# Kernel optimization log

Measured on AMD Instinct MI355X. Metric: run time of the kernel, lower is better.

## Reference

```python
import jax, jax.numpy as jnp
import numpy as np

EMBED_DIM = 1024
NUM_HEADS = 16
HEAD_DIM = EMBED_DIM // NUM_HEADS


def setup_inputs() -> dict:
    key = jax.random.key(0)
    kx, kw1, kb1, kw2, kb2 = jax.random.split(key, 5)
    B, T, C = 4, 2048, EMBED_DIM
    s = 1.0 / np.sqrt(C)
    return {
        "x": jax.random.normal(kx, (B, T, C), dtype=jnp.float32),
        "qkv_w": jax.random.uniform(kw1, (3 * C, C), jnp.float32, -s, s),
        "qkv_b": jax.random.uniform(kb1, (3 * C,), jnp.float32, -s, s),
        "out_w": jax.random.uniform(kw2, (C, C), jnp.float32, -s, s),
        "out_b": jax.random.uniform(kb2, (C,), jnp.float32, -s, s),
    }


def reference(x, qkv_w, qkv_b, out_w, out_b):
    B, T, C = x.shape
    H, D = NUM_HEADS, HEAD_DIM
    qkv = x @ qkv_w.T + qkv_b                      # [B,T,3C]
    qkv = qkv.reshape(B, T, 3, H, D)
    q = qkv[:, :, 0].transpose(0, 2, 1, 3)         # [B,H,T,D]
    k = qkv[:, :, 1].transpose(0, 2, 1, 3)
    v = qkv[:, :, 2].transpose(0, 2, 1, 3)
    att = jnp.einsum("bhqd,bhkd->bhqk", q, k) / jnp.sqrt(jnp.float32(D))
    causal = jnp.tril(jnp.ones((T, T), dtype=bool))
    att = jnp.where(causal, att, -jnp.inf)
    att = jax.nn.softmax(att, axis=-1)
    out = jnp.einsum("bhqk,bhkd->bhqd", att, v)    # [B,H,T,D]
    out = out.transpose(0, 2, 1, 3).reshape(B, T, C)
    return out @ out_w.T + out_b
```

## Files before the change

kernel.cpp:

```cpp
#include <hip/hip_runtime.h>
#include <stdint.h>

typedef _Float16 f16;
typedef _Float16 f16x2 __attribute__((ext_vector_type(2)));
typedef _Float16 f16x4 __attribute__((ext_vector_type(4)));
typedef _Float16 f16x8 __attribute__((ext_vector_type(8)));
typedef float f32x4 __attribute__((ext_vector_type(4)));
typedef float f32x16 __attribute__((ext_vector_type(16)));
typedef unsigned int u32;
typedef unsigned int u32x4 __attribute__((ext_vector_type(4)));
typedef int i32x2 __attribute__((ext_vector_type(2)));

#define LOG2E 1.44269504088896340736f

__device__ __forceinline__ f32x4 mfma_16x16x32(f16x8 a, f16x8 b, f32x4 c) {
    return __builtin_amdgcn_mfma_f32_16x16x32_f16(a, b, c, 0, 0, 0);
}
__device__ __forceinline__ f32x16 mfma_32x32x16(f16x8 a, f16x8 b, f32x16 c) {
    return __builtin_amdgcn_mfma_f32_32x32x16_f16(a, b, c, 0, 0, 0);
}

__device__ __forceinline__ void gload_lds16(const void* g, void* l) {
    __builtin_amdgcn_global_load_lds(
        (const __attribute__((address_space(1))) unsigned int*)g,
        (__attribute__((address_space(3))) unsigned int*)l, 16, 0, 0);
}

__device__ __forceinline__ void plswap_u32(u32& a, u32& b) {
    i32x2 r = __builtin_amdgcn_permlane32_swap((int)a, (int)b, false, false);
    a = (u32)r[0]; b = (u32)r[1];
}

__global__ void cast_f32_f16(const float* __restrict__ src, f16* __restrict__ dst, int n4) {
    int i = blockIdx.x * 256 + threadIdx.x;
    if (i >= n4) return;
    float4 v = reinterpret_cast<const float4*>(src)[i];
    f16x4 o;
    o[0] = (f16)v.x; o[1] = (f16)v.y; o[2] = (f16)v.z; o[3] = (f16)v.w;
    reinterpret_cast<f16x4*>(dst)[i] = o;
}

template<int MODE>
__global__ __launch_bounds__(256, 2)
void gemm_tn(const f16* __restrict__ A, const f16* __restrict__ W,
             const float* __restrict__ bias, void* __restrict__ outp,
             int M, int N, int K)
{
    __shared__ __align__(16) f16 As[128 * 32];
    __shared__ __align__(16) f16 Bs[128 * 32];

    const int lane = threadIdx.x & 63;
    const int wave = threadIdx.x >> 6;
    const int l15 = lane & 15, l4 = lane >> 4;

    const int nwg = (int)(gridDim.x * gridDim.y);
    int orig = (int)(blockIdx.y * gridDim.x + blockIdx.x);
    int cpx = nwg >> 3;
    int w = (orig & 7) * cpx + (orig >> 3);
    const int row0 = (w / (int)gridDim.x) * 128;
    const int col0 = (w % (int)gridDim.x) * 128;
    const int wr = wave >> 1, wc = wave & 1;

    f32x4 acc[4][4] = {};

    const int srow = lane >> 2;
    const int scol = (lane & 3) * 8;

    for (int k0 = 0; k0 < K; k0 += 32) {
        __syncthreads();
        #pragma unroll
        for (int it = 0; it < 2; ++it) {
            int chunk = it * 4 + wave;
            const f16* gA = A + (size_t)(row0 + chunk * 16 + srow) * K + k0 + scol;
            gload_lds16(gA, As + chunk * 512);
            const f16* gB = W + (size_t)(col0 + chunk * 16 + srow) * K + k0 + scol;
            gload_lds16(gB, Bs + chunk * 512);
        }
        __syncthreads();

        f16x8 af[4], bf[4];
        #pragma unroll
        for (int m = 0; m < 4; ++m)
            af[m] = *reinterpret_cast<const f16x8*>(As + (wr * 64 + m * 16 + l15) * 32 + l4 * 8);
        #pragma unroll
        for (int n = 0; n < 4; ++n)
            bf[n] = *reinterpret_cast<const f16x8*>(Bs + (wc * 64 + n * 16 + l15) * 32 + l4 * 8);
        #pragma unroll
        for (int m = 0; m < 4; ++m)
            #pragma unroll
            for (int n = 0; n < 4; ++n)
                acc[m][n] = mfma_16x16x32(af[m], bf[n], acc[m][n]);
    }

    if (MODE == 0) {
        f16* qb = (f16*)outp;
        const size_t HS = (size_t)64 * 2048 * 64;
        #pragma unroll
        for (int m = 0; m < 4; ++m) {
            int rbase = row0 + wr * 64 + m * 16 + l4 * 4;
            #pragma unroll
            for (int n = 0; n < 4; ++n) {
                int j = col0 + wc * 64 + n * 16 + l15;
                int which = j >> 10;
                int h = (j >> 6) & 15;
                int d = j & 63;
                float bj = bias[j];
                f16* base = qb + (size_t)which * HS;
                float scale = (which == 0) ? (0.125f * LOG2E) : 1.0f;
                #pragma unroll
                for (int r = 0; r < 4; ++r) {
                    int row = rbase + r;
                    int b = row >> 11, t = row & 2047;
                    size_t off = ((size_t)(b * 16 + h) * 2048 + t) * 64 + d;
                    base[off] = (f16)((acc[m][n][r] + bj) * scale);
                }
            }
        }
    } else {
        float* O = (float*)outp;
        #pragma unroll
        for (int m = 0; m < 4; ++m) {
            int rbase = row0 + wr * 64 + m * 16 + l4 * 4;
            #pragma unroll
            for (int n = 0; n < 4; ++n) {
                int j = col0 + wc * 64 + n * 16 + l15;
                float bj = bias[j];
                #pragma unroll
                for (int r = 0; r < 4; ++r)
                    O[(size_t)(rbase + r) * N + j] = acc[m][n][r] + bj;
            }
        }
    }
}

__global__ __launch_bounds__(256, 4)
void attn_kernel(const f16* __restrict__ qb, const f16* __restrict__ kb,
                 const f16* __restrict__ vb, f16* __restrict__ ob)
{
    __shared__ __align__(16) f16 Ks[2][4096];
    __shared__ __align__(16) f16 Vs[2][64][68];

    const int tid = (int)threadIdx.x;
    const int bh = (int)blockIdx.x;
    const int qblk = (int)gridDim.y - 1 - (int)blockIdx.y;
    const int lane = tid & 63;
    const int wave = tid >> 6;
    const int l31 = lane & 31;
    const int hi  = lane >> 5;
    const int q0 = qblk * 128;
    const int qw = q0 + wave * 32;

    const f16* Qp = qb + ((size_t)bh * 2048 + qw) * 64;
    f16x8 qf[4];
    #pragma unroll
    for (int ss = 0; ss < 4; ++ss)
        qf[ss] = *reinterpret_cast<const f16x8*>(Qp + l31 * 64 + ss * 16 + hi * 8);

    float Lr = 0.0f;
    f32x16 oacc[2] = {};

    const int ntiles = 2 * qblk + 2;
    const f16* Kbh = kb + (size_t)bh * 2048 * 64;
    const f16* Vbh = vb + (size_t)bh * 2048 * 64;

    f16x8 vld0, vld1;
    {
        #pragma unroll
        for (int it = 0; it < 2; ++it) {
            int c = it * 4 + wave;
            gload_lds16(Kbh + lane * 64 + c * 8, &Ks[0][0] + c * 512);
        }
        vld0 = *reinterpret_cast<const f16x8*>(Vbh + lane * 64 + (wave * 2 + 0) * 8);
        vld1 = *reinterpret_cast<const f16x8*>(Vbh + lane * 64 + (wave * 2 + 1) * 8);
    }

    for (int t = 0; t < ntiles; ++t) {
        const int cur = t & 1;
        const int kv0 = t * 64;

        #pragma unroll
        for (int it = 0; it < 2; ++it) {
            int dblk = wave * 2 + it;
            const f16x8 v = it ? vld1 : vld0;
            #pragma unroll
            for (int e = 0; e < 8; ++e)
                Vs[cur][dblk * 8 + e][lane] = v[e];
        }

        __syncthreads();

        {
            const int kvn = (t + 1 < ntiles) ? (t + 1) * 64 : t * 64;
            const f16* Ktn = Kbh + (size_t)kvn * 64;
            #pragma unroll
            for (int it = 0; it < 2; ++it) {
                int c = it * 4 + wave;
                gload_lds16(Ktn + lane * 64 + c * 8, &Ks[cur ^ 1][0] + c * 512);
            }
            const f16* Vtn = Vbh + (size_t)kvn * 64;
            vld0 = *reinterpret_cast<const f16x8*>(Vtn + lane * 64 + (wave * 2 + 0) * 8);
            vld1 = *reinterpret_cast<const f16x8*>(Vtn + lane * 64 + (wave * 2 + 1) * 8);
        }

        if (kv0 <= qw + 31) {
            const f16* Ksc = &Ks[cur][0];

            f32x16 s0 = {}, s1 = {};
            __builtin_amdgcn_s_setprio(1);
            #pragma unroll
            for (int ss = 0; ss < 4; ++ss) {
                f16x8 kf0 = *reinterpret_cast<const f16x8*>(Ksc + (2 * ss + hi) * 512 + l31 * 8);
                f16x8 kf1 = *reinterpret_cast<const f16x8*>(Ksc + (2 * ss + hi) * 512 + (32 + l31) * 8);
                s0 = mfma_32x32x16(kf0, qf[ss], s0);
                s1 = mfma_32x32x16(kf1, qf[ss], s1);
            }
            __builtin_amdgcn_s_setprio(0);

            if (kv0 + 63 > qw) {
                const int qg = qw + l31;
                #pragma unroll
                for (int r = 0; r < 16; ++r) {
                    int k0g = kv0 + (r & 3) + 8 * (r >> 2) + 4 * hi;
                    if (k0g > qg)      s0[r] = -1e30f;
                    if (k0g + 32 > qg) s1[r] = -1e30f;
                }
            }

            float e0[16], e1[16];
            #pragma unroll
            for (int r = 0; r < 16; ++r) {
                e0[r] = exp2f(s0[r] - 8.0f);
                e1[r] = exp2f(s1[r] - 8.0f);
            }
            float sm[16];
            #pragma unroll
            for (int i = 0; i < 16; ++i) sm[i] = e0[i] + e1[i];
            #pragma unroll
            for (int st = 8; st > 0; st >>= 1)
                #pragma unroll
                for (int i = 0; i < st; ++i) sm[i] += sm[i + st];
            float rs = sm[0];
            rs += __shfl_xor(rs, 32);
            Lr += rs;

            u32 cpk[2][8];
            #pragma unroll
            for (int B = 0; B < 4; ++B) {
                cpk[0][2 * B]     = __builtin_bit_cast(u32, __builtin_amdgcn_cvt_pkrtz(e0[4 * B],     e0[4 * B + 1]));
                cpk[0][2 * B + 1] = __builtin_bit_cast(u32, __builtin_amdgcn_cvt_pkrtz(e0[4 * B + 2], e0[4 * B + 3]));
                cpk[1][2 * B]     = __builtin_bit_cast(u32, __builtin_amdgcn_cvt_pkrtz(e1[4 * B],     e1[4 * B + 1]));
                cpk[1][2 * B + 1] = __builtin_bit_cast(u32, __builtin_amdgcn_cvt_pkrtz(e1[4 * B + 2], e1[4 * B + 3]));
            }

            __builtin_amdgcn_s_setprio(1);
            #pragma unroll
            for (int ss = 0; ss < 4; ++ss) {
                const int kbi = ss >> 1, qq = ss & 1;
                u32 a0 = cpk[kbi][4 * qq + 0], b0 = cpk[kbi][4 * qq + 2];
                u32 a1 = cpk[kbi][4 * qq + 1], b1 = cpk[kbi][4 * qq + 3];
                plswap_u32(a0, b0);
                plswap_u32(a1, b1);
                u32x4 up; up[0] = a0; up[1] = a1; up[2] = b0; up[3] = b1;
                f16x8 pa = __builtin_bit_cast(f16x8, up);
                #pragma unroll
                for (int db = 0; db < 2; ++db) {
                    const f16* vp = &Vs[cur][db * 32 + l31][16 * ss + 8 * hi];
                    f16x4 v0 = *reinterpret_cast<const f16x4*>(vp);
                    f16x4 v1 = *reinterpret_cast<const f16x4*>(vp + 4);
                    f16x8 vf = __builtin_shufflevector(v0, v1, 0, 1, 2, 3, 4, 5, 6, 7);
                    oacc[db] = mfma_32x32x16(pa, vf, oacc[db]);
                }
            }
            __builtin_amdgcn_s_setprio(0);
        }
    }

    float rcp = 1.0f / Lr;
    float rr[16];
    #pragma unroll
    for (int r = 0; r < 16; ++r)
        rr[r] = __shfl(rcp, (r & 3) + 8 * (r >> 2) + 4 * hi);

    const int b = bh >> 4, h = bh & 15;
    f16* O = ob + ((size_t)b * 2048 + qw) * 1024 + h * 64;
    #pragma unroll
    for (int db = 0; db < 2; ++db)
        #pragma unroll
        for (int r = 0; r < 16; ++r) {
            int q = (r & 3) + 8 * (r >> 2) + 4 * hi;
            O[(size_t)q * 1024 + db * 32 + l31] = (f16)(oacc[db][r] * rr[r]);
        }
}

extern "C" void kernel_launch(void* const* d_in, const int* in_sizes, int n_in,
                              void* d_out, int out_size, void* d_ws, size_t ws_size,
                              hipStream_t stream)
{
    const float* x    = (const float*)d_in[0];
    const float* qkvw = (const float*)d_in[1];
    const float* qkvb = (const float*)d_in[2];
    const float* outw = (const float*)d_in[3];
    const float* outb = (const float*)d_in[4];
    float* out = (float*)d_out;

    f16* x_h    = (f16*)d_ws;
    f16* qkvw_h = x_h + (size_t)8192 * 1024;
    f16* outw_h = qkvw_h + (size_t)3072 * 1024;
    f16* q_buf  = outw_h + (size_t)1024 * 1024;
    f16* att_o  = q_buf + (size_t)3 * 8388608;

    cast_f32_f16<<<8192, 256, 0, stream>>>(x, x_h, 2097152);
    cast_f32_f16<<<3072, 256, 0, stream>>>(qkvw, qkvw_h, 786432);
    cast_f32_f16<<<1024, 256, 0, stream>>>(outw, outw_h, 262144);

    gemm_tn<0><<<dim3(24, 64), 256, 0, stream>>>(x_h, qkvw_h, qkvb, q_buf, 8192, 3072, 1024);
    attn_kernel<<<dim3(64, 16), 256, 0, stream>>>(q_buf, q_buf + 8388608, q_buf + 2 * 8388608, att_o);
    gemm_tn<1><<<dim3(8, 64), 256, 0, stream>>>(att_o, outw_h, outb, out, 8192, 1024, 1024);
}
```

Baseline: 188.2 us.

## Pair low and high causal query blocks per attention workgroup; fuse cast kernels

Each attention workgroup now handles two query blocks, p and 15-p, so every block does the same amount of causal work. Both blocks share the K/V tiles already staged in LDS, which halves K/V loads per query and removes the tail imbalance. The cost is roughly double the accumulator and Q register use, so occupancy drops from 4 to 2 blocks per CU, and the grid shrinks to 512 blocks. The three fp32-to-fp16 cast launches are also merged into one kernel that picks its source by block index.

```diff
diff --git a/kernel.cpp b/kernel.cpp
--- a/kernel.cpp
+++ b/kernel.cpp
@@ -31,9 +31,16 @@
     a = (u32)r[0]; b = (u32)r[1];
 }
 
-__global__ void cast_f32_f16(const float* __restrict__ src, f16* __restrict__ dst, int n4) {
-    int i = blockIdx.x * 256 + threadIdx.x;
-    if (i >= n4) return;
+__global__ void cast_all(const float* __restrict__ x, const float* __restrict__ w1,
+                         const float* __restrict__ w2, f16* __restrict__ xo,
+                         f16* __restrict__ w1o, f16* __restrict__ w2o) {
+    int b = blockIdx.x;
+    const float* src;
+    f16* dst;
+    int i;
+    if (b < 8192)       { src = x;  dst = xo;  i = b * 256 + (int)threadIdx.x; }
+    else if (b < 11264) { src = w1; dst = w1o; i = (b - 8192) * 256 + (int)threadIdx.x; }
+    else                { src = w2; dst = w2o; i = (b - 11264) * 256 + (int)threadIdx.x; }
     float4 v = reinterpret_cast<const float4*>(src)[i];
     f16x4 o;
     o[0] = (f16)v.x; o[1] = (f16)v.y; o[2] = (f16)v.z; o[3] = (f16)v.w;
@@ -133,7 +140,7 @@
     }
 }
 
-__global__ __launch_bounds__(256, 4)
+__global__ __launch_bounds__(256, 2)
 void attn_kernel(const f16* __restrict__ qb, const f16* __restrict__ kb,
                  const f16* __restrict__ vb, f16* __restrict__ ob)
 {
@@ -142,24 +149,28 @@
 
     const int tid = (int)threadIdx.x;
     const int bh = (int)blockIdx.x;
-    const int qblk = (int)gridDim.y - 1 - (int)blockIdx.y;
+    const int p = (int)blockIdx.y;
+    const int qlo = p, qhi = 15 - p;
     const int lane = tid & 63;
     const int wave = tid >> 6;
     const int l31 = lane & 31;
     const int hi  = lane >> 5;
-    const int q0 = qblk * 128;
-    const int qw = q0 + wave * 32;
-
-    const f16* Qp = qb + ((size_t)bh * 2048 + qw) * 64;
-    f16x8 qf[4];
+
+    const int qwlo = qlo * 128 + wave * 32;
+    const int qwhi = qhi * 128 + wave * 32;
+
+    const f16* Qbh = qb + (size_t)bh * 2048 * 64;
+    f16x8 qflo[4], qfhi[4];
     #pragma unroll
-    for (int ss = 0; ss < 4; ++ss)
-        qf[ss] = *reinterpret_cast<const f16x8*>(Qp + l31 * 64 + ss * 16 + hi * 8);
-
-    float Lr = 0.0f;
-    f32x16 oacc[2] = {};
-
-    const int ntiles = 2 * qblk + 2;
+    for (int ss = 0; ss < 4; ++ss) {
+        qflo[ss] = *reinterpret_cast<const f16x8*>(Qbh + (size_t)(qwlo + l31) * 64 + ss * 16 + hi * 8);
+        qfhi[ss] = *reinterpret_cast<const f16x8*>(Qbh + (size_t)(qwhi + l31) * 64 + ss * 16 + hi * 8);
+    }
+
+    float Llo = 0.0f, Lhi = 0.0f;
+    f32x16 olo[2] = {}, ohi[2] = {};
+
+    const int ntiles = 2 * qhi + 2;
     const f16* Kbh = kb + (size_t)bh * 2048 * 64;
     const f16* Vbh = vb + (size_t)bh * 2048 * 64;
 
@@ -202,22 +213,34 @@
             vld1 = *reinterpret_cast<const f16x8*>(Vtn + lane * 64 + (wave * 2 + 1) * 8);
         }
 
-        if (kv0 <= qw + 31) {
-            const f16* Ksc = &Ks[cur][0];
-
-            f32x16 s0 = {}, s1 = {};
-            __builtin_amdgcn_s_setprio(1);
-            #pragma unroll
-            for (int ss = 0; ss < 4; ++ss) {
-                f16x8 kf0 = *reinterpret_cast<const f16x8*>(Ksc + (2 * ss + hi) * 512 + l31 * 8);
-                f16x8 kf1 = *reinterpret_cast<const f16x8*>(Ksc + (2 * ss + hi) * 512 + (32 + l31) * 8);
-                s0 = mfma_32x32x16(kf0, qf[ss], s0);
-                s1 = mfma_32x32x16(kf1, qf[ss], s1);
-            }
-            __builtin_amdgcn_s_setprio(0);
-
-            if (kv0 + 63 > qw) {
-                const int qg = qw + l31;
+        const bool do_hi = (kv0 <= qwhi + 31);
+        const bool do_lo = (kv0 <= qwlo + 31);
+        if (!(do_hi || do_lo)) continue;
+
+        const f16* Ksc = &Ks[cur][0];
+
+        f32x16 sh0 = {}, sh1 = {}, sl0 = {}, sl1 = {};
+        __builtin_amdgcn_s_setprio(1);
+        #pragma unroll
+        for (int ss = 0; ss < 4; ++ss) {
+            f16x8 kf0 = *reinterpret_cast<const f16x8*>(Ksc + (2 * ss + hi) * 512 + l31 * 8);
+            f16x8 kf1 = *reinterpret_cast<const f16x8*>(Ksc + (2 * ss + hi) * 512 + (32 + l31) * 8);
+            if (do_hi) {
+                sh0 = mfma_32x32x16(kf0, qfhi[ss], sh0);
+                sh1 = mfma_32x32x16(kf1, qfhi[ss], sh1);
+            }
+            if (do_lo) {
+                sl0 = mfma_32x32x16(kf0, qflo[ss], sl0);
+                sl1 = mfma_32x32x16(kf1, qflo[ss], sl1);
+            }
+        }
+        __builtin_amdgcn_s_setprio(0);
+
+        u32 cpkh[2][8], cpkl[2][8];
+        auto softmax_pack = [&](f32x16& s0, f32x16& s1, float& Lr,
+                                int qbase, u32 (&cpk)[2][8]) {
+            if (kv0 + 63 > qbase) {
+                const int qg = qbase + l31;
                 #pragma unroll
                 for (int r = 0; r < 16; ++r) {
                     int k0g = kv0 + (r & 3) + 8 * (r >> 2) + 4 * hi;
@@ -225,7 +248,6 @@
                     if (k0g + 32 > qg) s1[r] = -1e30f;
                 }
             }
-
             float e0[16], e1[16];
             #pragma unroll
             for (int r = 0; r < 16; ++r) {
@@ -242,8 +264,6 @@
             float rs = sm[0];
             rs += __shfl_xor(rs, 32);
             Lr += rs;
-
-            u32 cpk[2][8];
             #pragma unroll
             for (int B = 0; B < 4; ++B) {
                 cpk[0][2 * B]     = __builtin_bit_cast(u32, __builtin_amdgcn_cvt_pkrtz(e0[4 * B],     e0[4 * B + 1]));
@@ -251,45 +271,75 @@
                 cpk[1][2 * B]     = __builtin_bit_cast(u32, __builtin_amdgcn_cvt_pkrtz(e1[4 * B],     e1[4 * B + 1]));
                 cpk[1][2 * B + 1] = __builtin_bit_cast(u32, __builtin_amdgcn_cvt_pkrtz(e1[4 * B + 2], e1[4 * B + 3]));
             }
-
-            __builtin_amdgcn_s_setprio(1);
-            #pragma unroll
-            for (int ss = 0; ss < 4; ++ss) {
-                const int kbi = ss >> 1, qq = ss & 1;
-                u32 a0 = cpk[kbi][4 * qq + 0], b0 = cpk[kbi][4 * qq + 2];
-                u32 a1 = cpk[kbi][4 * qq + 1], b1 = cpk[kbi][4 * qq + 3];
+        };
+        if (do_hi) softmax_pack(sh0, sh1, Lhi, qwhi, cpkh);
+        if (do_lo) softmax_pack(sl0, sl1, Llo, qwlo, cpkl);
+
+        __builtin_amdgcn_s_setprio(1);
+        #pragma unroll
+        for (int ss = 0; ss < 4; ++ss) {
+            const int kbi = ss >> 1, qq = ss & 1;
+            f16x8 pah, pal;
+            if (do_hi) {
+                u32 a0 = cpkh[kbi][4 * qq + 0], b0 = cpkh[kbi][4 * qq + 2];
+                u32 a1 = cpkh[kbi][4 * qq + 1], b1 = cpkh[kbi][4 * qq + 3];
                 plswap_u32(a0, b0);
                 plswap_u32(a1, b1);
                 u32x4 up; up[0] = a0; up[1] = a1; up[2] = b0; up[3] = b1;
-                f16x8 pa = __builtin_bit_cast(f16x8, up);
-                #pragma unroll
-                for (int db = 0; db < 2; ++db) {
-                    const f16* vp = &Vs[cur][db * 32 + l31][16 * ss + 8 * hi];
-                    f16x4 v0 = *reinterpret_cast<const f16x4*>(vp);
-                    f16x4 v1 = *reinterpret_cast<const f16x4*>(vp + 4);
-                    f16x8 vf = __builtin_shufflevector(v0, v1, 0, 1, 2, 3, 4, 5, 6, 7);
-                    oacc[db] = mfma_32x32x16(pa, vf, oacc[db]);
-                }
-            }
-            __builtin_amdgcn_s_setprio(0);
-        }
-    }
-
-    float rcp = 1.0f / Lr;
-    float rr[16];
-    #pragma unroll
-    for (int r = 0; r < 16; ++r)
-        rr[r] = __shfl(rcp, (r & 3) + 8 * (r >> 2) + 4 * hi);
+                pah = __builtin_bit_cast(f16x8, up);
+            }
+            if (do_lo) {
+                u32 a0 = cpkl[kbi][4 * qq + 0], b0 = cpkl[kbi][4 * qq + 2];
+                u32 a1 = cpkl[kbi][4 * qq + 1], b1 = cpkl[kbi][4 * qq + 3];
+                plswap_u32(a0, b0);
+                plswap_u32(a1, b1);
+                u32x4 up; up[0] = a0; up[1] = a1; up[2] = b0; up[3] = b1;
+                pal = __builtin_bit_cast(f16x8, up);
+            }
+            #pragma unroll
+            for (int db = 0; db < 2; ++db) {
+                const f16* vp = &Vs[cur][db * 32 + l31][16 * ss + 8 * hi];
+                f16x4 v0 = *reinterpret_cast<const f16x4*>(vp);
+                f16x4 v1 = *reinterpret_cast<const f16x4*>(vp + 4);
+                f16x8 vf = __builtin_shufflevector(v0, v1, 0, 1, 2, 3, 4, 5, 6, 7);
+                if (do_hi) ohi[db] = mfma_32x32x16(pah, vf, ohi[db]);
+                if (do_lo) olo[db] = mfma_32x32x16(pal, vf, olo[db]);
+            }
+        }
+        __builtin_amdgcn_s_setprio(0);
+    }
 
     const int b = bh >> 4, h = bh & 15;
-    f16* O = ob + ((size_t)b * 2048 + qw) * 1024 + h * 64;
-    #pragma unroll
-    for (int db = 0; db < 2; ++db)
-        #pragma unroll
-        for (int r = 0; r < 16; ++r) {
-            int q = (r & 3) + 8 * (r >> 2) + 4 * hi;
-            O[(size_t)q * 1024 + db * 32 + l31] = (f16)(oacc[db][r] * rr[r]);
-        }
+    {
+        float rcp = 1.0f / Lhi;
+        float rr[16];
+        #pragma unroll
+        for (int r = 0; r < 16; ++r)
+            rr[r] = __shfl(rcp, (r & 3) + 8 * (r >> 2) + 4 * hi);
+        f16* O = ob + ((size_t)b * 2048 + qwhi) * 1024 + h * 64;
+        #pragma unroll
+        for (int db = 0; db < 2; ++db)
+            #pragma unroll
+            for (int r = 0; r < 16; ++r) {
+                int q = (r & 3) + 8 * (r >> 2) + 4 * hi;
+                O[(size_t)q * 1024 + db * 32 + l31] = (f16)(ohi[db][r] * rr[r]);
+            }
+    }
+    {
+        float rcp = 1.0f / Llo;
+        float rr[16];
+        #pragma unroll
+        for (int r = 0; r < 16; ++r)
+            rr[r] = __shfl(rcp, (r & 3) + 8 * (r >> 2) + 4 * hi);
+        f16* O = ob + ((size_t)b * 2048 + qwlo) * 1024 + h * 64;
+        #pragma unroll
+        for (int db = 0; db < 2; ++db)
+            #pragma unroll
+            for (int r = 0; r < 16; ++r) {
+                int q = (r & 3) + 8 * (r >> 2) + 4 * hi;
+                O[(size_t)q * 1024 + db * 32 + l31] = (f16)(olo[db][r] * rr[r]);
+            }
+    }
 }
 
 extern "C" void kernel_launch(void* const* d_in, const int* in_sizes, int n_in,
@@ -309,11 +359,9 @@
     f16* q_buf  = outw_h + (size_t)1024 * 1024;
     f16* att_o  = q_buf + (size_t)3 * 8388608;
 
-    cast_f32_f16<<<8192, 256, 0, stream>>>(x, x_h, 2097152);
-    cast_f32_f16<<<3072, 256, 0, stream>>>(qkvw, qkvw_h, 786432);
-    cast_f32_f16<<<1024, 256, 0, stream>>>(outw, outw_h, 262144);
+    cast_all<<<12288, 256, 0, stream>>>(x, qkvw, outw, x_h, qkvw_h, outw_h);
 
     gemm_tn<0><<<dim3(24, 64), 256, 0, stream>>>(x_h, qkvw_h, qkvb, q_buf, 8192, 3072, 1024);
-    attn_kernel<<<dim3(64, 16), 256, 0, stream>>>(q_buf, q_buf + 8388608, q_buf + 2 * 8388608, att_o);
+    attn_kernel<<<dim3(64, 8), 256, 0, stream>>>(q_buf, q_buf + 8388608, q_buf + 2 * 8388608, att_o);
     gemm_tn<1><<<dim3(8, 64), 256, 0, stream>>>(att_o, outw_h, outb, out, 8192, 1024, 1024);
 }
```

After: 195.4 us. 1.04x slower.

## Use persistent attention blocks with atomic work queue and fuse cast kernels

Applied to the files above, without the earlier changes.

The attention kernel becomes persistent: 768 blocks pull (q-block, head) jobs from a global atomic counter in order of longest causal work first, which balances the triangular workload across CUs. The three fp32-to-fp16 cast launches are merged into one kernel, and a memset resets the counter each call. The redundant prefetch on the last tile is also skipped. This adds an atomic and a barrier per job and one extra memset launch, and there is a possible LDS race when the next job's first K load overwrites buffer 0 while slow waves may still be reading it.

```diff
diff --git a/kernel.cpp b/kernel.cpp
--- a/kernel.cpp
+++ b/kernel.cpp
@@ -31,9 +31,16 @@
     a = (u32)r[0]; b = (u32)r[1];
 }
 
-__global__ void cast_f32_f16(const float* __restrict__ src, f16* __restrict__ dst, int n4) {
-    int i = blockIdx.x * 256 + threadIdx.x;
-    if (i >= n4) return;
+__global__ void cast_all(const float* __restrict__ x, const float* __restrict__ w1,
+                         const float* __restrict__ w2, f16* __restrict__ xo,
+                         f16* __restrict__ w1o, f16* __restrict__ w2o) {
+    int b = blockIdx.x;
+    const float* src;
+    f16* dst;
+    int i;
+    if (b < 8192)       { src = x;  dst = xo;  i = b * 256 + (int)threadIdx.x; }
+    else if (b < 11264) { src = w1; dst = w1o; i = (b - 8192) * 256 + (int)threadIdx.x; }
+    else                { src = w2; dst = w2o; i = (b - 11264) * 256 + (int)threadIdx.x; }
     float4 v = reinterpret_cast<const float4*>(src)[i];
     f16x4 o;
     o[0] = (f16)v.x; o[1] = (f16)v.y; o[2] = (f16)v.z; o[3] = (f16)v.w;
@@ -135,161 +142,171 @@
 
 __global__ __launch_bounds__(256, 4)
 void attn_kernel(const f16* __restrict__ qb, const f16* __restrict__ kb,
-                 const f16* __restrict__ vb, f16* __restrict__ ob)
+                 const f16* __restrict__ vb, f16* __restrict__ ob,
+                 u32* __restrict__ counter)
 {
     __shared__ __align__(16) f16 Ks[2][4096];
     __shared__ __align__(16) f16 Vs[2][64][68];
+    __shared__ int s_job;
 
     const int tid = (int)threadIdx.x;
-    const int bh = (int)blockIdx.x;
-    const int qblk = (int)gridDim.y - 1 - (int)blockIdx.y;
     const int lane = tid & 63;
     const int wave = tid >> 6;
     const int l31 = lane & 31;
     const int hi  = lane >> 5;
-    const int q0 = qblk * 128;
-    const int qw = q0 + wave * 32;
-
-    const f16* Qp = qb + ((size_t)bh * 2048 + qw) * 64;
-    f16x8 qf[4];
-    #pragma unroll
-    for (int ss = 0; ss < 4; ++ss)
-        qf[ss] = *reinterpret_cast<const f16x8*>(Qp + l31 * 64 + ss * 16 + hi * 8);
-
-    float Lr = 0.0f;
-    f32x16 oacc[2] = {};
-
-    const int ntiles = 2 * qblk + 2;
-    const f16* Kbh = kb + (size_t)bh * 2048 * 64;
-    const f16* Vbh = vb + (size_t)bh * 2048 * 64;
-
-    f16x8 vld0, vld1;
-    {
-        #pragma unroll
-        for (int it = 0; it < 2; ++it) {
-            int c = it * 4 + wave;
-            gload_lds16(Kbh + lane * 64 + c * 8, &Ks[0][0] + c * 512);
-        }
-        vld0 = *reinterpret_cast<const f16x8*>(Vbh + lane * 64 + (wave * 2 + 0) * 8);
-        vld1 = *reinterpret_cast<const f16x8*>(Vbh + lane * 64 + (wave * 2 + 1) * 8);
-    }
-
-    for (int t = 0; t < ntiles; ++t) {
-        const int cur = t & 1;
-        const int kv0 = t * 64;
-
-        #pragma unroll
-        for (int it = 0; it < 2; ++it) {
-            int dblk = wave * 2 + it;
-            const f16x8 v = it ? vld1 : vld0;
-            #pragma unroll
-            for (int e = 0; e < 8; ++e)
-                Vs[cur][dblk * 8 + e][lane] = v[e];
-        }
-
+
+    for (;;) {
+        if (tid == 0) s_job = (int)atomicAdd(counter, 1u);
         __syncthreads();
-
+        const int j = s_job;
+        if (j >= 1024) return;
+
+        const int qblk = 15 - (j >> 6);
+        const int bh = j & 63;
+        const int q0 = qblk * 128;
+        const int qw = q0 + wave * 32;
+
+        const f16* Qp = qb + ((size_t)bh * 2048 + qw) * 64;
+        f16x8 qf[4];
+        #pragma unroll
+        for (int ss = 0; ss < 4; ++ss)
+            qf[ss] = *reinterpret_cast<const f16x8*>(Qp + l31 * 64 + ss * 16 + hi * 8);
+
+        float Lr = 0.0f;
+        f32x16 oacc[2] = {};
+
+        const int ntiles = 2 * qblk + 2;
+        const f16* Kbh = kb + (size_t)bh * 2048 * 64;
+        const f16* Vbh = vb + (size_t)bh * 2048 * 64;
+
+        f16x8 vld0, vld1;
         {
-            const int kvn = (t + 1 < ntiles) ? (t + 1) * 64 : t * 64;
-            const f16* Ktn = Kbh + (size_t)kvn * 64;
             #pragma unroll
             for (int it = 0; it < 2; ++it) {
                 int c = it * 4 + wave;
-                gload_lds16(Ktn + lane * 64 + c * 8, &Ks[cur ^ 1][0] + c * 512);
-            }
-            const f16* Vtn = Vbh + (size_t)kvn * 64;
-            vld0 = *reinterpret_cast<const f16x8*>(Vtn + lane * 64 + (wave * 2 + 0) * 8);
-            vld1 = *reinterpret_cast<const f16x8*>(Vtn + lane * 64 + (wave * 2 + 1) * 8);
-        }
-
-        if (kv0 <= qw + 31) {
-            const f16* Ksc = &Ks[cur][0];
-
-            f32x16 s0 = {}, s1 = {};
-            __builtin_amdgcn_s_setprio(1);
-            #pragma unroll
-            for (int ss = 0; ss < 4; ++ss) {
-                f16x8 kf0 = *reinterpret_cast<const f16x8*>(Ksc + (2 * ss + hi) * 512 + l31 * 8);
-                f16x8 kf1 = *reinterpret_cast<const f16x8*>(Ksc + (2 * ss + hi) * 512 + (32 + l31) * 8);
-                s0 = mfma_32x32x16(kf0, qf[ss], s0);
-                s1 = mfma_32x32x16(kf1, qf[ss], s1);
-            }
-            __builtin_amdgcn_s_setprio(0);
-
-            if (kv0 + 63 > qw) {
-                const int qg = qw + l31;
+                gload_lds16(Kbh + lane * 64 + c * 8, &Ks[0][0] + c * 512);
+            }
+            vld0 = *reinterpret_cast<const f16x8*>(Vbh + lane * 64 + (wave * 2 + 0) * 8);
+            vld1 = *reinterpret_cast<const f16x8*>(Vbh + lane * 64 + (wave * 2 + 1) * 8);
+        }
+
+        for (int t = 0; t < ntiles; ++t) {
+            const int cur = t & 1;
+            const int kv0 = t * 64;
+
+            #pragma unroll
+            for (int it = 0; it < 2; ++it) {
+                int dblk = wave * 2 + it;
+                const f16x8 v = it ? vld1 : vld0;
+                #pragma unroll
+                for (int e = 0; e < 8; ++e)
+                    Vs[cur][dblk * 8 + e][lane] = v[e];
+            }
+
+            __syncthreads();
+
+            if (t + 1 < ntiles) {
+                const int kvn = (t + 1) * 64;
+                const f16* Ktn = Kbh + (size_t)kvn * 64;
+                #pragma unroll
+                for (int it = 0; it < 2; ++it) {
+                    int c = it * 4 + wave;
+                    gload_lds16(Ktn + lane * 64 + c * 8, &Ks[cur ^ 1][0] + c * 512);
+                }
+                const f16* Vtn = Vbh + (size_t)kvn * 64;
+                vld0 = *reinterpret_cast<const f16x8*>(Vtn + lane * 64 + (wave * 2 + 0) * 8);
+                vld1 = *reinterpret_cast<const f16x8*>(Vtn + lane * 64 + (wave * 2 + 1) * 8);
+            }
+
+            if (kv0 <= qw + 31) {
+                const f16* Ksc = &Ks[cur][0];
+
+                f32x16 s0 = {}, s1 = {};
+                __builtin_amdgcn_s_setprio(1);
+                #pragma unroll
+                for (int ss = 0; ss < 4; ++ss) {
+                    f16x8 kf0 = *reinterpret_cast<const f16x8*>(Ksc + (2 * ss + hi) * 512 + l31 * 8);
+                    f16x8 kf1 = *reinterpret_cast<const f16x8*>(Ksc + (2 * ss + hi) * 512 + (32 + l31) * 8);
+                    s0 = mfma_32x32x16(kf0, qf[ss], s0);
+                    s1 = mfma_32x32x16(kf1, qf[ss], s1);
+                }
+                __builtin_amdgcn_s_setprio(0);
+
+                if (kv0 + 63 > qw) {
+                    const int qg = qw + l31;
+                    #pragma unroll
+                    for (int r = 0; r < 16; ++r) {
+                        int k0g = kv0 + (r & 3) + 8 * (r >> 2) + 4 * hi;
+                        if (k0g > qg)      s0[r] = -1e30f;
+                        if (k0g + 32 > qg) s1[r] = -1e30f;
+                    }
+                }
+
+                float e0[16], e1[16];
                 #pragma unroll
                 for (int r = 0; r < 16; ++r) {
-                    int k0g = kv0 + (r & 3) + 8 * (r >> 2) + 4 * hi;
-                    if (k0g > qg)      s0[r] = -1e30f;
-                    if (k0g + 32 > qg) s1[r] = -1e30f;
-                }
-            }
-
-            float e0[16], e1[16];
+                    e0[r] = exp2f(s0[r] - 8.0f);
+                    e1[r] = exp2f(s1[r] - 8.0f);
+                }
+                float sm[16];
+                #pragma unroll
+                for (int i = 0; i < 16; ++i) sm[i] = e0[i] + e1[i];
+                #pragma unroll
+                for (int st = 8; st > 0; st >>= 1)
+                    #pragma unroll
+                    for (int i = 0; i < st; ++i) sm[i] += sm[i + st];
+                float rs = sm[0];
+                rs += __shfl_xor(rs, 32);
+                Lr += rs;
+
+                u32 cpk[2][8];
+                #pragma unroll
+                for (int B = 0; B < 4; ++B) {
+                    cpk[0][2 * B]     = __builtin_bit_cast(u32, __builtin_amdgcn_cvt_pkrtz(e0[4 * B],     e0[4 * B + 1]));
+                    cpk[0][2 * B + 1] = __builtin_bit_cast(u32, __builtin_amdgcn_cvt_pkrtz(e0[4 * B + 2], e0[4 * B + 3]));
+                    cpk[1][2 * B]     = __builtin_bit_cast(u32, __builtin_amdgcn_cvt_pkrtz(e1[4 * B],     e1[4 * B + 1]));
+                    cpk[1][2 * B + 1] = __builtin_bit_cast(u32, __builtin_amdgcn_cvt_pkrtz(e1[4 * B + 2], e1[4 * B + 3]));
+                }
+
+                __builtin_amdgcn_s_setprio(1);
+                #pragma unroll
+                for (int ss = 0; ss < 4; ++ss) {
+                    const int kbi = ss >> 1, qq = ss & 1;
+                    u32 a0 = cpk[kbi][4 * qq + 0], b0 = cpk[kbi][4 * qq + 2];
+                    u32 a1 = cpk[kbi][4 * qq + 1], b1 = cpk[kbi][4 * qq + 3];
+                    plswap_u32(a0, b0);
+                    plswap_u32(a1, b1);
+                    u32x4 up; up[0] = a0; up[1] = a1; up[2] = b0; up[3] = b1;
+                    f16x8 pa = __builtin_bit_cast(f16x8, up);
+                    #pragma unroll
+                    for (int db = 0; db < 2; ++db) {
+                        const f16* vp = &Vs[cur][db * 32 + l31][16 * ss + 8 * hi];
+                        f16x4 v0 = *reinterpret_cast<const f16x4*>(vp);
+                        f16x4 v1 = *reinterpret_cast<const f16x4*>(vp + 4);
+                        f16x8 vf = __builtin_shufflevector(v0, v1, 0, 1, 2, 3, 4, 5, 6, 7);
+                        oacc[db] = mfma_32x32x16(pa, vf, oacc[db]);
+                    }
+                }
+                __builtin_amdgcn_s_setprio(0);
+            }
+        }
+
+        float rcp = 1.0f / Lr;
+        float rr[16];
+        #pragma unroll
+        for (int r = 0; r < 16; ++r)
+            rr[r] = __shfl(rcp, (r & 3) + 8 * (r >> 2) + 4 * hi);
+
+        const int b = bh >> 4, h = bh & 15;
+        f16* O = ob + ((size_t)b * 2048 + qw) * 1024 + h * 64;
+        #pragma unroll
+        for (int db = 0; db < 2; ++db)
             #pragma unroll
             for (int r = 0; r < 16; ++r) {
-                e0[r] = exp2f(s0[r] - 8.0f);
-                e1[r] = exp2f(s1[r] - 8.0f);
-            }
-            float sm[16];
-            #pragma unroll
-            for (int i = 0; i < 16; ++i) sm[i] = e0[i] + e1[i];
-            #pragma unroll
-            for (int st = 8; st > 0; st >>= 1)
-                #pragma unroll
-                for (int i = 0; i < st; ++i) sm[i] += sm[i + st];
-            float rs = sm[0];
-            rs += __shfl_xor(rs, 32);
-            Lr += rs;
-
-            u32 cpk[2][8];
-            #pragma unroll
-            for (int B = 0; B < 4; ++B) {
-                cpk[0][2 * B]     = __builtin_bit_cast(u32, __builtin_amdgcn_cvt_pkrtz(e0[4 * B],     e0[4 * B + 1]));
-                cpk[0][2 * B + 1] = __builtin_bit_cast(u32, __builtin_amdgcn_cvt_pkrtz(e0[4 * B + 2], e0[4 * B + 3]));
-                cpk[1][2 * B]     = __builtin_bit_cast(u32, __builtin_amdgcn_cvt_pkrtz(e1[4 * B],     e1[4 * B + 1]));
-                cpk[1][2 * B + 1] = __builtin_bit_cast(u32, __builtin_amdgcn_cvt_pkrtz(e1[4 * B + 2], e1[4 * B + 3]));
-            }
-
-            __builtin_amdgcn_s_setprio(1);
-            #pragma unroll
-            for (int ss = 0; ss < 4; ++ss) {
-                const int kbi = ss >> 1, qq = ss & 1;
-                u32 a0 = cpk[kbi][4 * qq + 0], b0 = cpk[kbi][4 * qq + 2];
-                u32 a1 = cpk[kbi][4 * qq + 1], b1 = cpk[kbi][4 * qq + 3];
-                plswap_u32(a0, b0);
-                plswap_u32(a1, b1);
-                u32x4 up; up[0] = a0; up[1] = a1; up[2] = b0; up[3] = b1;
-                f16x8 pa = __builtin_bit_cast(f16x8, up);
-                #pragma unroll
-                for (int db = 0; db < 2; ++db) {
-                    const f16* vp = &Vs[cur][db * 32 + l31][16 * ss + 8 * hi];
-                    f16x4 v0 = *reinterpret_cast<const f16x4*>(vp);
-                    f16x4 v1 = *reinterpret_cast<const f16x4*>(vp + 4);
-                    f16x8 vf = __builtin_shufflevector(v0, v1, 0, 1, 2, 3, 4, 5, 6, 7);
-                    oacc[db] = mfma_32x32x16(pa, vf, oacc[db]);
-                }
-            }
-            __builtin_amdgcn_s_setprio(0);
-        }
+                int q = (r & 3) + 8 * (r >> 2) + 4 * hi;
+                O[(size_t)q * 1024 + db * 32 + l31] = (f16)(oacc[db][r] * rr[r]);
+            }
     }
-
-    float rcp = 1.0f / Lr;
-    float rr[16];
-    #pragma unroll
-    for (int r = 0; r < 16; ++r)
-        rr[r] = __shfl(rcp, (r & 3) + 8 * (r >> 2) + 4 * hi);
-
-    const int b = bh >> 4, h = bh & 15;
-    f16* O = ob + ((size_t)b * 2048 + qw) * 1024 + h * 64;
-    #pragma unroll
-    for (int db = 0; db < 2; ++db)
-        #pragma unroll
-        for (int r = 0; r < 16; ++r) {
-            int q = (r & 3) + 8 * (r >> 2) + 4 * hi;
-            O[(size_t)q * 1024 + db * 32 + l31] = (f16)(oacc[db][r] * rr[r]);
-        }
 }
 
 extern "C" void kernel_launch(void* const* d_in, const int* in_sizes, int n_in,
@@ -308,12 +325,12 @@
     f16* outw_h = qkvw_h + (size_t)3072 * 1024;
     f16* q_buf  = outw_h + (size_t)1024 * 1024;
     f16* att_o  = q_buf + (size_t)3 * 8388608;
-
-    cast_f32_f16<<<8192, 256, 0, stream>>>(x, x_h, 2097152);
-    cast_f32_f16<<<3072, 256, 0, stream>>>(qkvw, qkvw_h, 786432);
-    cast_f32_f16<<<1024, 256, 0, stream>>>(outw, outw_h, 262144);
+    u32* counter = (u32*)(att_o + (size_t)8192 * 1024);
+
+    hipMemsetAsync(counter, 0, 4, stream);
+    cast_all<<<12288, 256, 0, stream>>>(x, qkvw, outw, x_h, qkvw_h, outw_h);
 
     gemm_tn<0><<<dim3(24, 64), 256, 0, stream>>>(x_h, qkvw_h, qkvb, q_buf, 8192, 3072, 1024);
-    attn_kernel<<<dim3(64, 16), 256, 0, stream>>>(q_buf, q_buf + 8388608, q_buf + 2 * 8388608, att_o);
+    attn_kernel<<<768, 256, 0, stream>>>(q_buf, q_buf + 8388608, q_buf + 2 * 8388608, att_o, counter);
     gemm_tn<1><<<dim3(8, 64), 256, 0, stream>>>(att_o, outw_h, outb, out, 8192, 1024, 1024);
 }
```

New measurement: 199.3 us. +5.9%, slower.
